# Kernel tuning notes

Measured on AMD Instinct MI355X. Metric: run time of the kernel, lower is better.

The kernel has to match this reference:

```python
import math
import jax, jax.numpy as jnp
import numpy as np

H = 64; W = 64; SX = 2; SY = 2; RATIO = 0.5; HEADS = 8


def _tome_indices(metric):
    # no_rand variant of bipartite_soft_matching_random2d: dst token is the
    # top-left element of every (SY, SX) block; indices computed under stop_gradient
    # (torch.no_grad in the original).
    m = jax.lax.stop_gradient(metric)
    B, N, _ = m.shape
    hsy, wsx = H // SY, W // SX
    num_dst = hsy * wsx
    dst_mask = ((jnp.arange(H)[:, None] % SY == 0) & (jnp.arange(W)[None, :] % SX == 0)).reshape(-1)
    order = jnp.argsort(jnp.where(dst_mask, -1, 0), stable=True)  # -1 entries (dst) first
    b_idx, a_idx = order[:num_dst], order[num_dst:]               # [num_dst], [N-num_dst]
    mn = m / jnp.linalg.norm(m, axis=-1, keepdims=True)
    a, b = mn[:, a_idx], mn[:, b_idx]
    scores = jnp.einsum('bsc,bdc->bsd', a, b)                      # [B, Ns, Nd] cosine sims
    r = min(a.shape[1], int(N * RATIO))
    node_max = scores.max(-1)
    node_idx = scores.argmax(-1)
    edge_idx = jnp.argsort(-node_max, axis=-1, stable=True)        # descending
    unm_idx, src_idx = edge_idx[:, r:], edge_idx[:, :r]
    dst_idx = jnp.take_along_axis(node_idx, src_idx, axis=1)
    return a_idx, b_idx, unm_idx, src_idx, dst_idx


def _merge(x, idxs):
    a_idx, b_idx, unm_idx, src_idx, dst_idx = idxs
    src, dst = x[:, a_idx], x[:, b_idx]
    unm = jnp.take_along_axis(src, unm_idx[..., None], axis=1)
    s = jnp.take_along_axis(src, src_idx[..., None], axis=1)
    bg = jnp.broadcast_to(jnp.arange(x.shape[0])[:, None], dst_idx.shape)
    sums = jnp.zeros_like(dst).at[bg, dst_idx].add(s)
    counts = jnp.zeros(dst.shape[:2], x.dtype).at[bg, dst_idx].add(1.0)
    dst = (dst + sums) / (1.0 + counts[..., None])  # scatter_reduce 'mean', include_self
    return jnp.concatenate([unm, dst], axis=1)


def _unmerge(x, idxs, N):
    a_idx, b_idx, unm_idx, src_idx, dst_idx = idxs
    unm_len = unm_idx.shape[1]
    unm, dst = x[:, :unm_len], x[:, unm_len:]
    s = jnp.take_along_axis(dst, dst_idx[..., None], axis=1)
    B, _, c = x.shape
    out = jnp.zeros((B, N, c), x.dtype)
    out = out.at[:, b_idx].set(dst)
    bgu = jnp.broadcast_to(jnp.arange(B)[:, None], unm_idx.shape)
    out = out.at[bgu, a_idx[unm_idx]].set(unm)
    bgs = jnp.broadcast_to(jnp.arange(B)[:, None], src_idx.shape)
    out = out.at[bgs, a_idx[src_idx]].set(s)
    return out


def _ln(x, g, b):
    mu = x.mean(-1, keepdims=True)
    var = ((x - mu) ** 2).mean(-1, keepdims=True)
    return (x - mu) / jnp.sqrt(var + 1e-5) * g + b


def _attn(x, ctx, wq, wk, wv, wo, bo):
    B, Nq, C = x.shape
    dh = C // HEADS
    q = (x @ wq).reshape(B, Nq, HEADS, dh)
    k = (ctx @ wk).reshape(B, -1, HEADS, dh)
    v = (ctx @ wv).reshape(B, -1, HEADS, dh)
    s = jnp.einsum('bqhd,bkhd->bhqk', q, k) * (1.0 / math.sqrt(dh))
    p = jax.nn.softmax(s, axis=-1)
    o = jnp.einsum('bhqk,bkhd->bqhd', p, v).reshape(B, Nq, C)
    return o @ wo + bo


def _forward(net, context, ln1_g, ln1_b, ln2_g, ln2_b, ln3_g, ln3_b,
             attn1_wq, attn1_wk, attn1_wv, attn1_wo, attn1_bo,
             attn2_wq, attn2_wk, attn2_wv, attn2_wo, attn2_bo,
             ff_w1, ff_b1, ff_w2, ff_b2):
    N = net.shape[1]
    idxs = _tome_indices(net)
    # self-attn with ToMe merge/unmerge (merge_attn=True)
    xm = _merge(_ln(net, ln1_g, ln1_b), idxs)
    net = _unmerge(_attn(xm, xm, attn1_wq, attn1_wk, attn1_wv, attn1_wo, attn1_bo), idxs, N) + net
    # cross-attn (merge_crossattn=False)
    net = _attn(_ln(net, ln2_g, ln2_b), context, attn2_wq, attn2_wk, attn2_wv, attn2_wo, attn2_bo) + net
    # GEGLU feed-forward (merge_mlp=False)
    h1 = _ln(net, ln3_g, ln3_b) @ ff_w1 + ff_b1
    xh, gh = jnp.split(h1, 2, axis=-1)
    net = (xh * jax.nn.gelu(gh, approximate=False)) @ ff_w2 + ff_b2 + net
    return net


def setup_inputs() -> dict:
    key = jax.random.key(0)
    ks = jax.random.split(key, 12)
    B, N, C, Lc, Dc = 2, 4096, 320, 77, 768
    dff = 4 * C
    w = lambda k, s: jax.random.normal(k, s, jnp.float32) * 0.02
    return {
        'net': jax.random.normal(ks[0], (B, N, C), jnp.float32),
        'context': jax.random.normal(ks[1], (B, Lc, Dc), jnp.float32),
        'ln1_g': jnp.ones((C,), jnp.float32), 'ln1_b': jnp.zeros((C,), jnp.float32),
        'ln2_g': jnp.ones((C,), jnp.float32), 'ln2_b': jnp.zeros((C,), jnp.float32),
        'ln3_g': jnp.ones((C,), jnp.float32), 'ln3_b': jnp.zeros((C,), jnp.float32),
        'attn1_wq': w(ks[2], (C, C)), 'attn1_wk': w(ks[3], (C, C)),
        'attn1_wv': w(ks[4], (C, C)), 'attn1_wo': w(ks[5], (C, C)),
        'attn1_bo': jnp.zeros((C,), jnp.float32),
        'attn2_wq': w(ks[6], (C, C)), 'attn2_wk': w(ks[7], (Dc, C)),
        'attn2_wv': w(ks[8], (Dc, C)), 'attn2_wo': w(ks[9], (C, C)),
        'attn2_bo': jnp.zeros((C,), jnp.float32),
        'ff_w1': w(ks[10], (C, 2 * dff)), 'ff_b1': jnp.zeros((2 * dff,), jnp.float32),
        'ff_w2': w(ks[11], (dff, C)), 'ff_b2': jnp.zeros((C,), jnp.float32),
    }


def reference(net, context, ln1_g, ln1_b, ln2_g, ln2_b, ln3_g, ln3_b,
              attn1_wq, attn1_wk, attn1_wv, attn1_wo, attn1_bo,
              attn2_wq, attn2_wk, attn2_wv, attn2_wo, attn2_bo,
              ff_w1, ff_b1, ff_w2, ff_b2):
    return _forward(net, context, ln1_g, ln1_b, ln2_g, ln2_b, ln3_g, ln3_b,
                    attn1_wq, attn1_wk, attn1_wv, attn1_wo, attn1_bo,
                    attn2_wq, attn2_wk, attn2_wv, attn2_wo, attn2_bo,
                    ff_w1, ff_b1, ff_w2, ff_b2)
```

## Files before the change

kernel.cpp:

```cpp
#include <hip/hip_runtime.h>

typedef __attribute__((ext_vector_type(8))) short bf16x8;
typedef __attribute__((ext_vector_type(4))) float f32x4;

constexpr int kB   = 2;
constexpr int kN   = 4096;
constexpr int kC   = 320;
constexpr int kNA  = 3072;
constexpr int kNB  = 1024;
constexpr int kNM  = 2048;
constexpr int kR   = 2048;
constexpr int kH   = 8;
constexpr int kDH  = 40;
constexpr int kLC  = 77;
constexpr int kDC  = 768;
constexpr int kDFF = 1280;

__device__ __forceinline__ unsigned short f2b(float f){
  unsigned u = __float_as_uint(f);
  u += 0x7FFF + ((u>>16)&1);
  return (unsigned short)(u>>16);
}
__device__ __forceinline__ float b2f(unsigned short h){ return __uint_as_float(((unsigned)h)<<16); }

__device__ __forceinline__ float wave_sum(float v){
  #pragma unroll
  for (int m=32;m>=1;m>>=1) v += __shfl_xor(v, m, 64);
  return v;
}
__device__ __forceinline__ int d_arank(int h, int w){
  int base = 32*((h+1)>>1) + 64*(h>>1);
  return base + ((h&1) ? w : (w>>1));
}

constexpr size_t rndB(size_t x){ return (x + 255) & ~(size_t)255; }
constexpr size_t B_mnA  = 0;
constexpr size_t B_mnB  = rndB(B_mnA + (size_t)kB*kNA*kC*4);
constexpr size_t B_y32  = rndB(B_mnB + (size_t)kB*kNB*kC*4);
constexpr size_t B_xm   = rndB(B_y32 + (size_t)kB*kN*kC*4);
constexpr size_t B_xo1  = rndB(B_xm  + (size_t)kB*kNM*kC*4);
constexpr size_t B_net1 = rndB(B_xo1 + (size_t)kB*kNM*kC*4);
constexpr size_t B_H    = 0;
constexpr size_t B_net2 = rndB(B_net1 + (size_t)kB*kN*kC*4);
constexpr size_t B_G    = rndB(B_net2 + (size_t)kB*kN*kC*4);
constexpr size_t B_QKb  = rndB(B_G    + (size_t)kB*kN*kDFF*2);
constexpr size_t B_Vtg  = rndB(B_QKb  + (size_t)kB*kNM*640*2);
constexpr size_t B_yb   = rndB(B_Vtg  + (size_t)320*kB*kNM*2);
constexpr size_t B_xmb  = rndB(B_yb   + (size_t)kB*kN*kC*2);
constexpr size_t B_Ao1b = rndB(B_xmb  + (size_t)kB*kNM*kC*2);
constexpr size_t B_Q2b  = rndB(B_Ao1b + (size_t)kB*kNM*kC*2);
constexpr size_t B_Ao2b = rndB(B_Q2b  + (size_t)kB*kN*kC*2);
constexpr size_t B_KV2b = rndB(B_Ao2b + (size_t)kB*kN*kC*2);
constexpr size_t B_Vt2g = rndB(B_KV2b + (size_t)kB*kLC*640*2);
constexpr size_t B_ctxb = rndB(B_Vt2g + (size_t)kB*320*80*2);
constexpr size_t B_Wqkv = rndB(B_ctxb + (size_t)kB*kLC*kDC*2);
constexpr size_t B_Wo1  = rndB(B_Wqkv + (size_t)960*320*2);
constexpr size_t B_Wq2  = rndB(B_Wo1  + (size_t)320*320*2);
constexpr size_t B_Wkv2 = rndB(B_Wq2  + (size_t)320*320*2);
constexpr size_t B_Wo2  = rndB(B_Wkv2 + (size_t)640*768*2);
constexpr size_t B_Wff1 = rndB(B_Wo2  + (size_t)320*320*2);
constexpr size_t B_Wff2 = rndB(B_Wff1 + (size_t)2560*320*2);
constexpr size_t B_cnt  = rndB(B_Wff2 + (size_t)320*1280*2);
constexpr size_t B_pack = rndB(B_cnt  + (size_t)kB*kNB*4);
constexpr size_t B_rank = rndB(B_pack + (size_t)kB*kNA*8);
constexpr size_t B_nidx = rndB(B_rank + (size_t)kB*kNA*4);
constexpr size_t B_mrg  = rndB(B_nidx + (size_t)kB*kNA*4);
constexpr size_t B_slot = rndB(B_mrg  + (size_t)kB*kNA*4);
constexpr size_t B_unml = rndB(B_slot + (size_t)kB*kNA*4);
constexpr size_t B_ucnt = rndB(B_unml + (size_t)kB*kNB*4);
constexpr size_t B_aidx = rndB(B_ucnt + 64);
constexpr size_t B_Op   = rndB(B_aidx + (size_t)kNA*4);
constexpr size_t B_lp   = rndB(B_Op   + (size_t)2*4096*320*4);

__global__ void k_gather(const float* __restrict__ net, float* __restrict__ mA, float* __restrict__ mB,
                         unsigned long long* __restrict__ pack, int* __restrict__ ucnt,
                         int* __restrict__ a_idx, int* __restrict__ rank){
  int blk = blockIdx.x; int b = blk >> 12; int t = blk & 4095;
  int lane = threadIdx.x;
  int gid = blk*64 + lane;
  if (gid < kB*kNA){ pack[gid] = 0ull; rank[gid] = 0; }
  if (gid < kB) ucnt[gid] = 0;
  if (gid < kN){
    int h = gid>>6, w = gid&63;
    if ((h|w)&1) a_idx[d_arank(h,w)] = gid;
  }
  const float* xp = net + ((size_t)b*kN + t)*kC;
  float v[5]; float s2 = 0.f;
  #pragma unroll
  for (int i=0;i<5;i++){ float f = xp[lane + i*64]; v[i]=f; s2 += f*f; }
  s2 = wave_sum(s2);
  float rn = 1.0f / sqrtf(s2);
  int h=t>>6, w=t&63;
  float* dp;
  if (!((h|w)&1)) dp = mB + ((size_t)b*kNB + ((h>>1)*32+(w>>1)))*kC;
  else            dp = mA + ((size_t)b*kNA + d_arank(h,w))*kC;
  #pragma unroll
  for (int i=0;i<5;i++) dp[lane + i*64] = v[i]*rn;
}

__global__ __launch_bounds__(256) void k_scores(const float* __restrict__ mA, const float* __restrict__ mB,
                                                unsigned long long* __restrict__ pack){
  __shared__ __align__(16) float As[16][136];
  __shared__ __align__(16) float Bs[16][68];
  const int b = blockIdx.z;
  const int m0 = blockIdx.x*128, n0 = blockIdx.y*64;
  const int tid = threadIdx.x;
  const int mr = tid>>4, nc = tid&15;
  const float* Ab = mA + (size_t)b*kNA*kC;
  const float* Bb = mB + (size_t)b*kNB*kC;
  float acc[8][4] = {};
  const int ar = tid>>1, ac8 = (tid&1)*8;
  const int br = tid>>2, bc4 = (tid&3)*4;
  for (int k0=0; k0<kC; k0+=16){
    __syncthreads();
    {
      float4 a0 = *reinterpret_cast<const float4*>(&Ab[(size_t)(m0+ar)*kC + k0 + ac8]);
      float4 a1 = *reinterpret_cast<const float4*>(&Ab[(size_t)(m0+ar)*kC + k0 + ac8 + 4]);
      As[ac8+0][ar]=a0.x; As[ac8+1][ar]=a0.y; As[ac8+2][ar]=a0.z; As[ac8+3][ar]=a0.w;
      As[ac8+4][ar]=a1.x; As[ac8+5][ar]=a1.y; As[ac8+6][ar]=a1.z; As[ac8+7][ar]=a1.w;
      float4 bv = *reinterpret_cast<const float4*>(&Bb[(size_t)(n0+br)*kC + k0 + bc4]);
      Bs[bc4+0][br]=bv.x; Bs[bc4+1][br]=bv.y; Bs[bc4+2][br]=bv.z; Bs[bc4+3][br]=bv.w;
    }
    __syncthreads();
    #pragma unroll
    for (int kk=0;kk<16;kk++){
      const float4 a4a = *reinterpret_cast<const float4*>(&As[kk][mr*8]);
      const float4 a4b = *reinterpret_cast<const float4*>(&As[kk][mr*8+4]);
      const float4 b4  = *reinterpret_cast<const float4*>(&Bs[kk][nc*4]);
      const float aa[8]={a4a.x,a4a.y,a4a.z,a4a.w,a4b.x,a4b.y,a4b.z,a4b.w};
      const float bb[4]={b4.x,b4.y,b4.z,b4.w};
      #pragma unroll
      for (int i=0;i<8;i++)
        #pragma unroll
        for (int j=0;j<4;j++)
          acc[i][j] = fmaf(aa[i], bb[j], acc[i][j]);
    }
  }
  #pragma unroll
  for (int i=0;i<8;i++){
    float bs = acc[i][0]; int bj = n0 + nc*4;
    #pragma unroll
    for (int j=1;j<4;j++){
      float v = acc[i][j];
      if (v > bs){ bs=v; bj=n0+nc*4+j; }
    }
    #pragma unroll
    for (int off=1; off<16; off<<=1){
      float os = __shfl_xor(bs, off, 16);
      int   oj = __shfl_xor(bj, off, 16);
      if (os > bs || (os == bs && oj < bj)){ bs=os; bj=oj; }
    }
    if (nc == 0){
      unsigned int u = __float_as_uint(bs);
      unsigned int key = (u & 0x80000000u) ? ~u : (u | 0x80000000u);
      unsigned long long pk = ((unsigned long long)key << 32) |
                              (unsigned long long)(0xFFFFFFFFu - (unsigned int)bj);
      atomicMax(&pack[(size_t)b*kNA + m0 + mr*8 + i], pk);
    }
  }
}
__global__ __launch_bounds__(256) void k_rank_part(const unsigned long long* __restrict__ pack,
                                                   int* __restrict__ rank){
  __shared__ unsigned int keys[256];
  const int b = blockIdx.z;
  const int i = blockIdx.x*256 + threadIdx.x;
  const int j0 = blockIdx.y*256;
  const unsigned long long* pb = pack + (size_t)b*kNA;
  keys[threadIdx.x] = (unsigned int)(pb[j0 + threadIdx.x]>>32);
  unsigned int ki = (unsigned int)(pb[i]>>32);
  __syncthreads();
  int cnt = 0;
  #pragma unroll 8
  for (int jj=0;jj<256;jj++){
    unsigned int kj = keys[jj];
    int j = j0 + jj;
    cnt += (kj > ki) || (kj == ki && j < i);
  }
  atomicAdd(&rank[(size_t)b*kNA + i], cnt);
}
__global__ void k_rank_assign(const unsigned long long* __restrict__ pack, const int* __restrict__ rank,
                              int* __restrict__ node_idx, int* __restrict__ merged,
                              int* __restrict__ slot_of, int* __restrict__ unm_list,
                              int* __restrict__ ucnt){
  int b = blockIdx.y;
  int i = blockIdx.x*256 + threadIdx.x;
  unsigned long long p = pack[(size_t)b*kNA + i];
  node_idx[(size_t)b*kNA + i] = (int)(0xFFFFFFFFu - (unsigned int)(p & 0xFFFFFFFFull));
  int mg = rank[(size_t)b*kNA + i] < kR;
  merged[(size_t)b*kNA + i] = mg;
  if (!mg){
    int s = atomicAdd(&ucnt[b], 1);
    unm_list[(size_t)b*kNB + s] = i;
    slot_of[(size_t)b*kNA + i] = s;
  }
}

template<bool OB>
__global__ void k_ln(const float* __restrict__ x, const float* __restrict__ g,
                     const float* __restrict__ be, void* __restrict__ yv){
  const int row = blockIdx.x;
  const int lane = threadIdx.x;
  const float* xp = x + (size_t)row*kC;
  float v[5]; float s=0.f, s2=0.f;
  #pragma unroll
  for (int i=0;i<5;i++){ float f = xp[lane + i*64]; v[i]=f; s+=f; s2+=f*f; }
  s = wave_sum(s); s2 = wave_sum(s2);
  float mu = s * (1.0f/kC);
  float var = s2 * (1.0f/kC) - mu*mu;
  float rstd = rsqrtf(var + 1e-5f);
  #pragma unroll
  for (int i=0;i<5;i++){
    int c = lane + i*64;
    float o = (v[i]-mu)*rstd*g[c] + be[c];
    if (OB) ((unsigned short*)yv)[(size_t)row*kC + c] = f2b(o);
    else    ((float*)yv)[(size_t)row*kC + c] = o;
  }
}

__global__ void k_merge_ud(const float* __restrict__ y, const int* __restrict__ a_idx,
                           const int* __restrict__ unm_list, unsigned short* __restrict__ xmb,
                           float* __restrict__ xm, float* __restrict__ cnt){
  int blk = blockIdx.x;
  int lane = threadIdx.x;
  if (blk < kB*kNB){
    int b = blk >> 10; int s = blk & 1023;
    int i = unm_list[(size_t)b*kNB + s];
    int t = a_idx[i];
    const float* sp = y + ((size_t)b*kN + t)*kC;
    unsigned short* dp = xmb + ((size_t)b*kNM + s)*kC;
    #pragma unroll
    for (int q=0;q<5;q++) dp[lane+q*64] = f2b(sp[lane+q*64]);
  } else {
    blk -= kB*kNB;
    int b = blk >> 10; int j = blk & 1023;
    int t = 128*(j>>5) + 2*(j&31);
    const float* sp = y + ((size_t)b*kN + t)*kC;
    float* dp = xm + ((size_t)b*kNM + kNB + j)*kC;
    #pragma unroll
    for (int q=0;q<5;q++) dp[lane+q*64] = sp[lane+q*64];
    if (lane==0) cnt[(size_t)b*kNB + j] = 1.0f;
  }
}
__global__ void k_merge_src(const float* __restrict__ y, const int* __restrict__ a_idx,
                            const int* __restrict__ merged, const int* __restrict__ node_idx,
                            float* __restrict__ xm, float* __restrict__ cnt){
  int blk = blockIdx.x; int b = blk / kNA; int i = blk % kNA;
  if (!merged[(size_t)b*kNA + i]) return;
  int t = a_idx[i]; int j = node_idx[(size_t)b*kNA + i];
  const float* sp = y + ((size_t)b*kN + t)*kC;
  float* dp = xm + ((size_t)b*kNM + kNB + j)*kC;
  int lane = threadIdx.x;
  #pragma unroll
  for (int q=0;q<5;q++) atomicAdd(&dp[lane+q*64], sp[lane+q*64]);
  if (lane==0) atomicAdd(&cnt[(size_t)b*kNB + j], 1.0f);
}
__global__ void k_merge_scale(const float* __restrict__ xm, const float* __restrict__ cnt,
                              unsigned short* __restrict__ xmb){
  int blk = blockIdx.x; int b = blk >> 10; int j = blk & 1023;
  float inv = 1.0f / cnt[(size_t)b*kNB + j];
  const float* sp = xm + ((size_t)b*kNM + kNB + j)*kC;
  unsigned short* dp = xmb + ((size_t)b*kNM + kNB + j)*kC;
  int lane = threadIdx.x;
  #pragma unroll
  for (int q=0;q<5;q++) dp[lane+q*64] = f2b(sp[lane+q*64]*inv);
}

__global__ __launch_bounds__(256) void k_wt_all(
    const float* __restrict__ w0, const float* __restrict__ w1, const float* __restrict__ w2,
    const float* __restrict__ w3, const float* __restrict__ w4, const float* __restrict__ w5,
    const float* __restrict__ w6, const float* __restrict__ w7, const float* __restrict__ w8,
    const float* __restrict__ w9,
    unsigned short* __restrict__ Wqkv, unsigned short* __restrict__ Wo1,
    unsigned short* __restrict__ Wq2,  unsigned short* __restrict__ Wkv2,
    unsigned short* __restrict__ Wo2,  unsigned short* __restrict__ Wff1,
    unsigned short* __restrict__ Wff2,
    const float* __restrict__ ctx, unsigned short* __restrict__ ctxb,
    unsigned short* __restrict__ Vt2){
  const int bid = blockIdx.x;
  const int tid = threadIdx.x;
  if (bid >= 570){
    int base = (bid-570)*2048 + tid*8;
    #pragma unroll
    for (int j=0;j<8;j++){
      int i = base + j;
      if (i < kB*kLC*kDC) ctxb[i] = f2b(ctx[i]);
    }
    if (bid == 570){
      for (int r=tid; r<kB*320; r+=256){
        Vt2[(size_t)r*80 + 77] = 0; Vt2[(size_t)r*80 + 78] = 0; Vt2[(size_t)r*80 + 79] = 0;
      }
    }
    return;
  }
  const int jb[11]   = {0,25,50,75,100,125,185,245,270,470,570};
  const float* srcs[10] = {w0,w1,w2,w3,w4,w5,w6,w7,w8,w9};
  unsigned short* dsts[10] = {Wqkv, Wqkv+320*320, Wqkv+640*320, Wo1, Wq2,
                              Wkv2, Wkv2+320*768, Wo2, Wff1, Wff2};
  const int Kd[10] = {320,320,320,320,320,768,768,320,320,1280};
  const int Nd[10] = {320,320,320,320,320,320,320,320,2560,320};
  int job = 0;
  while (bid >= jb[job+1]) job++;
  int local = bid - jb[job];
  const int Nt = (Nd[job]+63)>>6;
  int k0 = (local / Nt)*64, n0 = (local % Nt)*64;
  const float* W = srcs[job];
  unsigned short* Wt = dsts[job];
  const int K = Kd[job], N = Nd[job];
  __shared__ float tile[64][65];
  #pragma unroll
  for (int l=0;l<16;l++){
    int e = tid + l*256; int r = e>>6, c = e&63;
    int gk = k0+r, gn = n0+c;
    tile[r][c] = (gk<K && gn<N) ? W[(size_t)gk*N+gn] : 0.f;
  }
  __syncthreads();
  #pragma unroll
  for (int l=0;l<16;l++){
    int e = tid + l*256; int r = e>>6, c = e&63;
    int gn = n0+r, gk = k0+c;
    if (gn<N && gk<K) Wt[(size_t)gn*K+gk] = f2b(tile[c][r]);
  }
}

template<typename OT, bool BIAS, bool RES, int SVM>
__global__ __launch_bounds__(256) void k_bgemm(const unsigned short* __restrict__ A,
    const unsigned short* __restrict__ Bt, const float* __restrict__ bias,
    const float* __restrict__ resid, OT* __restrict__ out, unsigned short* __restrict__ vt,
    int M, int N, int K, int ldo){
  constexpr int LDK = 72;
  __shared__ unsigned short As[128*LDK];
  __shared__ unsigned short Bs[128*LDK];
  const int tid = threadIdx.x;
  const int m0 = blockIdx.x*128, n0 = blockIdx.y*128;
  const int wid = tid>>6, lane = tid&63;
  const int wm = (wid>>1)*64, wn = (wid&1)*64;
  const int lr = lane&15, quad = lane>>4;
  const f32x4 zero4 = {0.f,0.f,0.f,0.f};
  f32x4 acc[4][4];
  #pragma unroll
  for (int i=0;i<4;i++)
    #pragma unroll
    for (int j=0;j<4;j++) acc[i][j] = zero4;
  for (int k0=0; k0<K; k0+=64){
    __syncthreads();
    #pragma unroll
    for (int l=0;l<4;l++){
      int e = tid + l*256;
      int row = e>>3, seg = (e&7)*8;
      int gm = m0+row;
      uint4 va = (gm<M) ? *reinterpret_cast<const uint4*>(&A[(size_t)gm*K + k0 + seg])
                        : make_uint4(0u,0u,0u,0u);
      *reinterpret_cast<uint4*>(&As[row*LDK + seg]) = va;
      int gn = n0+row;
      uint4 vb = (gn<N) ? *reinterpret_cast<const uint4*>(&Bt[(size_t)gn*K + k0 + seg])
                        : make_uint4(0u,0u,0u,0u);
      *reinterpret_cast<uint4*>(&Bs[row*LDK + seg]) = vb;
    }
    __syncthreads();
    #pragma unroll
    for (int kk=0; kk<64; kk+=32){
      bf16x8 af[4], bfr[4];
      #pragma unroll
      for (int i=0;i<4;i++) af[i]  = *reinterpret_cast<const bf16x8*>(&As[(wm+i*16+lr)*LDK + kk + quad*8]);
      #pragma unroll
      for (int j=0;j<4;j++) bfr[j] = *reinterpret_cast<const bf16x8*>(&Bs[(wn+j*16+lr)*LDK + kk + quad*8]);
      #pragma unroll
      for (int i=0;i<4;i++)
        #pragma unroll
        for (int j=0;j<4;j++)
          acc[i][j] = __builtin_amdgcn_mfma_f32_16x16x32_bf16(af[i], bfr[j], acc[i][j], 0, 0, 0);
    }
  }
  #pragma unroll
  for (int i=0;i<4;i++){
    #pragma unroll
    for (int j=0;j<4;j++){
      int gn = n0 + wn + j*16 + lr;
      if (gn >= N) continue;
      float bv = BIAS ? bias[gn] : 0.f;
      #pragma unroll
      for (int r=0;r<4;r++){
        int gm = m0 + wm + i*16 + quad*4 + r;
        if (gm >= M) continue;
        float v = acc[i][j][r] + bv;
        if (RES) v += resid[(size_t)gm*ldo + gn];
        if (SVM == 1 && gn >= 640){
          vt[(size_t)(gn-640)*4096 + gm] = f2b(v);
        } else if (SVM == 2 && gn >= 320){
          int bb = gm / 77, tok = gm - bb*77;
          vt[((size_t)bb*320 + (gn-320))*80 + tok] = f2b(v);
        } else {
          if constexpr (sizeof(OT)==2) out[(size_t)gm*ldo + gn] = (OT)f2b(v);
          else                         out[(size_t)gm*ldo + gn] = (OT)v;
        }
      }
    }
  }
}

template<typename OT, bool BIAS, bool RES, int SVM>
__global__ __launch_bounds__(256) void k_bgemm64(const unsigned short* __restrict__ A,
    const unsigned short* __restrict__ Bt, const float* __restrict__ bias,
    const float* __restrict__ resid, OT* __restrict__ out, unsigned short* __restrict__ vt,
    int M, int N, int K, int ldo){
  constexpr int LDK = 72;
  __shared__ unsigned short As[64*LDK];
  __shared__ unsigned short Bs[64*LDK];
  const int tid = threadIdx.x;
  const int m0 = blockIdx.x*64, n0 = blockIdx.y*64;
  const int wid = tid>>6, lane = tid&63;
  const int wm = (wid>>1)*32, wn = (wid&1)*32;
  const int lr = lane&15, quad = lane>>4;
  const f32x4 zero4 = {0.f,0.f,0.f,0.f};
  f32x4 acc[2][2];
  #pragma unroll
  for (int i=0;i<2;i++)
    #pragma unroll
    for (int j=0;j<2;j++) acc[i][j] = zero4;
  for (int k0=0; k0<K; k0+=64){
    __syncthreads();
    #pragma unroll
    for (int l=0;l<2;l++){
      int e = tid + l*256;
      int row = e>>3, seg = (e&7)*8;
      int gm = m0+row;
      uint4 va = (gm<M) ? *reinterpret_cast<const uint4*>(&A[(size_t)gm*K + k0 + seg])
                        : make_uint4(0u,0u,0u,0u);
      *reinterpret_cast<uint4*>(&As[row*LDK + seg]) = va;
      int gn = n0+row;
      uint4 vb = (gn<N) ? *reinterpret_cast<const uint4*>(&Bt[(size_t)gn*K + k0 + seg])
                        : make_uint4(0u,0u,0u,0u);
      *reinterpret_cast<uint4*>(&Bs[row*LDK + seg]) = vb;
    }
    __syncthreads();
    #pragma unroll
    for (int kk=0; kk<64; kk+=32){
      bf16x8 af[2], bfr[2];
      #pragma unroll
      for (int i=0;i<2;i++) af[i]  = *reinterpret_cast<const bf16x8*>(&As[(wm+i*16+lr)*LDK + kk + quad*8]);
      #pragma unroll
      for (int j=0;j<2;j++) bfr[j] = *reinterpret_cast<const bf16x8*>(&Bs[(wn+j*16+lr)*LDK + kk + quad*8]);
      #pragma unroll
      for (int i=0;i<2;i++)
        #pragma unroll
        for (int j=0;j<2;j++)
          acc[i][j] = __builtin_amdgcn_mfma_f32_16x16x32_bf16(af[i], bfr[j], acc[i][j], 0, 0, 0);
    }
  }
  #pragma unroll
  for (int i=0;i<2;i++){
    #pragma unroll
    for (int j=0;j<2;j++){
      int gn = n0 + wn + j*16 + lr;
      if (gn >= N) continue;
      float bv = BIAS ? bias[gn] : 0.f;
      #pragma unroll
      for (int r=0;r<4;r++){
        int gm = m0 + wm + i*16 + quad*4 + r;
        if (gm >= M) continue;
        float v = acc[i][j][r] + bv;
        if (RES) v += resid[(size_t)gm*ldo + gn];
        if (SVM == 1 && gn >= 640){
          vt[(size_t)(gn-640)*4096 + gm] = f2b(v);
        } else if (SVM == 2 && gn >= 320){
          int bb = gm / 77, tok = gm - bb*77;
          vt[((size_t)bb*320 + (gn-320))*80 + tok] = f2b(v);
        } else {
          if constexpr (sizeof(OT)==2) out[(size_t)gm*ldo + gn] = (OT)f2b(v);
          else                         out[(size_t)gm*ldo + gn] = (OT)v;
        }
      }
    }
  }
}

__global__ void k_geglu(const unsigned short* __restrict__ H, unsigned short* __restrict__ G){
  int e = blockIdx.x*256 + threadIdx.x;
  int m = e/160, t = e - m*160;
  const unsigned short* hp = H + (size_t)m*2560 + t*8;
  uint4 xv = *reinterpret_cast<const uint4*>(hp);
  uint4 gv = *reinterpret_cast<const uint4*>(hp + 1280);
  const unsigned short* xu = reinterpret_cast<const unsigned short*>(&xv);
  const unsigned short* gu = reinterpret_cast<const unsigned short*>(&gv);
  unsigned short ov[8];
  #pragma unroll
  for (int d=0; d<8; d++){
    float x = b2f(xu[d]);
    float g = b2f(gu[d]);
    float ge = 0.5f*g*(1.0f + erff(g*0.70710678118654752f));
    ov[d] = f2b(x*ge);
  }
  *reinterpret_cast<uint4*>(G + (size_t)m*1280 + t*8) = *reinterpret_cast<const uint4*>(ov);
}

__global__ __launch_bounds__(256) void k_attn1(const unsigned short* __restrict__ QK,
                                               const unsigned short* __restrict__ Vtg,
                                               float* __restrict__ Opart,
                                               float* __restrict__ lpart){
  constexpr int LP = 72, LV = 136;
  __shared__ unsigned short Ks[128*LP];
  __shared__ unsigned short Vt[48*LV];
  __shared__ unsigned short Ps[64*LV];
  const int b = blockIdx.z, hh = blockIdx.y;
  const int bx = blockIdx.x;
  const int q0 = (bx>>1)*64, kz = bx&1;
  const int tid = threadIdx.x;
  const int wid = tid>>6, lane = tid&63;
  const int lr = lane&15, quad = lane>>4;
  const int wm = wid*16;
  const float scale = 0.15811388300841898f;
  const unsigned short* Kb = QK + ((size_t)b*kNM)*640 + 320 + hh*kDH;
  const unsigned short* Vb = Vtg + (size_t)hh*kDH*4096 + (size_t)b*kNM;
  const uint4 z4 = make_uint4(0u,0u,0u,0u);
  const unsigned short* Qrow = QK + ((size_t)b*kNM + q0 + wm + lr)*640 + hh*kDH;
  bf16x8 aq0 = *reinterpret_cast<const bf16x8*>(Qrow + quad*8);
  bf16x8 aq1 = {0,0,0,0,0,0,0,0};
  if (quad == 0) aq1 = *reinterpret_cast<const bf16x8*>(Qrow + 32);
  for (int e=tid; e<384; e+=256){
    int row=e/3, seg=40+(e%3)*8;
    *reinterpret_cast<uint4*>(&Ks[row*LP+seg]) = z4;
  }
  for (int e=tid; e<136; e+=256){
    int row=40+e/17, seg=(e%17)*8;
    *reinterpret_cast<uint4*>(&Vt[row*LV+seg]) = z4;
  }
  const f32x4 zf = {0.f,0.f,0.f,0.f};
  f32x4 oacc[3] = {zf, zf, zf};
  float l_i[4] = {0.f, 0.f, 0.f, 0.f};
  const int kbeg = kz*1024, kend = kbeg + 1024;
  for (int kt=kbeg; kt<kend; kt+=128){
    __syncthreads();
    for (int e=tid; e<640; e+=256){
      int row=e/5, seg=(e%5)*8;
      *reinterpret_cast<uint4*>(&Ks[row*LP+seg]) =
        *reinterpret_cast<const uint4*>(Kb + (size_t)(kt+row)*640 + seg);
    }
    for (int e=tid; e<640; e+=256){
      int d=e>>4, seg=(e&15)*8;
      *reinterpret_cast<uint4*>(&Vt[d*LV+seg]) =
        *reinterpret_cast<const uint4*>(Vb + (size_t)d*4096 + kt + seg);
    }
    __syncthreads();
    f32x4 sacc[8];
    #pragma unroll
    for (int j=0;j<8;j++){
      bf16x8 bk0 = *reinterpret_cast<const bf16x8*>(&Ks[(j*16+lr)*LP + quad*8]);
      sacc[j] = __builtin_amdgcn_mfma_f32_16x16x32_bf16(aq0, bk0, zf, 0,0,0);
      bf16x8 bk1 = *reinterpret_cast<const bf16x8*>(&Ks[(j*16+lr)*LP + 32 + quad*8]);
      sacc[j] = __builtin_amdgcn_mfma_f32_16x16x32_bf16(aq1, bk1, sacc[j], 0,0,0);
    }
    #pragma unroll
    for (int r=0;r<4;r++){
      int row = wm + quad*4 + r;
      float psum = 0.f;
      #pragma unroll
      for (int j=0;j<8;j++){
        float p = __expf(sacc[j][r]*scale);
        psum += p;
        Ps[row*LV + j*16 + lr] = f2b(p);
      }
      #pragma unroll
      for (int off=1; off<16; off<<=1) psum += __shfl_xor(psum, off, 64);
      l_i[r] += psum;
    }
    #pragma unroll
    for (int s=0;s<4;s++){
      bf16x8 ap = *reinterpret_cast<const bf16x8*>(&Ps[(wm+lr)*LV + s*32 + quad*8]);
      #pragma unroll
      for (int nt=0;nt<3;nt++){
        bf16x8 bv = *reinterpret_cast<const bf16x8*>(&Vt[(nt*16+lr)*LV + s*32 + quad*8]);
        oacc[nt] = __builtin_amdgcn_mfma_f32_16x16x32_bf16(ap, bv, oacc[nt], 0,0,0);
      }
    }
  }
  float* Op = Opart + (size_t)kz*4096*320;
  float* lp = lpart + (size_t)kz*4096*8;
  #pragma unroll
  for (int r=0;r<4;r++){
    int grow = b*kNM + q0 + wm + quad*4 + r;
    #pragma unroll
    for (int nt=0;nt<3;nt++){
      int d = nt*16 + lr;
      if (d < kDH) Op[(size_t)grow*320 + hh*kDH + d] = oacc[nt][r];
    }
    if (lr == 0) lp[(size_t)grow*8 + hh] = l_i[r];
  }
}

__global__ void k_acomb(const float* __restrict__ Opart, const float* __restrict__ lpart,
                        unsigned short* __restrict__ Ao1b){
  int row = blockIdx.x;
  int lane = threadIdx.x;
  const float* o0 = Opart + (size_t)row*320;
  const float* o1 = Opart + (size_t)2*4096*320/2 + (size_t)row*320;
  const float* l0 = lpart + (size_t)row*8;
  const float* l1 = lpart + (size_t)4096*8 + (size_t)row*8;
  #pragma unroll
  for (int i=0;i<5;i++){
    int c = lane + i*64;
    int h = c/kDH;
    float v = (o0[c] + o1[c]) / (l0[h] + l1[h]);
    Ao1b[(size_t)row*320 + c] = f2b(v);
  }
}

__global__ __launch_bounds__(256) void k_attn2m(const unsigned short* __restrict__ Q,
                                                const unsigned short* __restrict__ KV,
                                                const unsigned short* __restrict__ Vt2,
                                                unsigned short* __restrict__ Oa){
  constexpr int LP = 72, LP2 = 104;
  __shared__ unsigned short Qs[64*LP];
  __shared__ unsigned short Ks[80*LP];
  __shared__ unsigned short Vts[48*LP2];
  __shared__ unsigned short Ps[64*LP2];
  const int b = blockIdx.z, hh = blockIdx.y;
  const int q0 = blockIdx.x*64;
  const int tid = threadIdx.x;
  const int wid = tid>>6, lane = tid&63;
  const int lr = lane&15, quad = lane>>4;
  const int wm = wid*16;
  const float scale = 0.15811388300841898f;
  const uint4 z4 = make_uint4(0u,0u,0u,0u);
  for (int e=tid; e<576; e+=256) *reinterpret_cast<uint4*>(&Qs[e*8]) = z4;
  for (int e=tid; e<720; e+=256) *reinterpret_cast<uint4*>(&Ks[e*8]) = z4;
  for (int e=tid; e<624; e+=256) *reinterpret_cast<uint4*>(&Vts[e*8]) = z4;
  for (int e=tid; e<832; e+=256) *reinterpret_cast<uint4*>(&Ps[e*8]) = z4;
  __syncthreads();
  for (int e=tid; e<320; e+=256){
    int row=e/5, seg=(e%5)*8;
    *reinterpret_cast<uint4*>(&Qs[row*LP+seg]) =
      *reinterpret_cast<const uint4*>(Q + ((size_t)b*kN + q0 + row)*kC + hh*kDH + seg);
  }
  for (int e=tid; e<385; e+=256){
    int row=e/5, seg=(e%5)*8;
    *reinterpret_cast<uint4*>(&Ks[row*LP+seg]) =
      *reinterpret_cast<const uint4*>(KV + ((size_t)b*kLC + row)*640 + hh*kDH + seg);
  }
  for (int e=tid; e<400; e+=256){
    int d=e/10, seg=(e%10)*8;
    *reinterpret_cast<uint4*>(&Vts[d*LP2+seg]) =
      *reinterpret_cast<const uint4*>(Vt2 + ((size_t)b*320 + hh*kDH + d)*80 + seg);
  }
  __syncthreads();
  const f32x4 zf = {0.f,0.f,0.f,0.f};
  f32x4 sacc[5] = {zf, zf, zf, zf, zf};
  bf16x8 aq0 = *reinterpret_cast<const bf16x8*>(&Qs[(wm+lr)*LP + quad*8]);
  bf16x8 aq1 = *reinterpret_cast<const bf16x8*>(&Qs[(wm+lr)*LP + 32 + quad*8]);
  #pragma unroll
  for (int j=0;j<5;j++){
    bf16x8 bk0 = *reinterpret_cast<const bf16x8*>(&Ks[(j*16+lr)*LP + quad*8]);
    sacc[j] = __builtin_amdgcn_mfma_f32_16x16x32_bf16(aq0, bk0, sacc[j], 0,0,0);
    bf16x8 bk1 = *reinterpret_cast<const bf16x8*>(&Ks[(j*16+lr)*LP + 32 + quad*8]);
    sacc[j] = __builtin_amdgcn_mfma_f32_16x16x32_bf16(aq1, bk1, sacc[j], 0,0,0);
  }
  float l_i[4];
  #pragma unroll
  for (int r=0;r<4;r++){
    float vv[5];
    float rm = -1e30f;
    #pragma unroll
    for (int j=0;j<5;j++){
      int c = j*16 + lr;
      vv[j] = sacc[j][r]*scale;
      if (c < kLC) rm = fmaxf(rm, vv[j]);
    }
    #pragma unroll
    for (int off=1; off<16; off<<=1) rm = fmaxf(rm, __shfl_xor(rm, off, 64));
    float psum = 0.f;
    int row = wm + quad*4 + r;
    #pragma unroll
    for (int j=0;j<5;j++){
      int c = j*16 + lr;
      float p = (c < kLC) ? __expf(vv[j]-rm) : 0.f;
      psum += p;
      Ps[row*LP2 + c] = f2b(p);
    }
    #pragma unroll
    for (int off=1; off<16; off<<=1) psum += __shfl_xor(psum, off, 64);
    l_i[r] = psum;
  }
  f32x4 oacc[3] = {zf, zf, zf};
  #pragma unroll
  for (int s=0;s<3;s++){
    bf16x8 ap = *reinterpret_cast<const bf16x8*>(&Ps[(wm+lr)*LP2 + s*32 + quad*8]);
    #pragma unroll
    for (int nt=0;nt<3;nt++){
      bf16x8 bv = *reinterpret_cast<const bf16x8*>(&Vts[(nt*16+lr)*LP2 + s*32 + quad*8]);
      oacc[nt] = __builtin_amdgcn_mfma_f32_16x16x32_bf16(ap, bv, oacc[nt], 0,0,0);
    }
  }
  #pragma unroll
  for (int r=0;r<4;r++){
    float inv = 1.0f / l_i[r];
    unsigned short* Ob = Oa + ((size_t)b*kN + q0 + wm + quad*4 + r)*kC + hh*kDH;
    #pragma unroll
    for (int nt=0;nt<3;nt++){
      int d = nt*16 + lr;
      if (d < kDH) Ob[d] = f2b(oacc[nt][r]*inv);
    }
  }
}

__global__ void k_unmerge(const float* __restrict__ net, const float* __restrict__ Xo,
                          const int* __restrict__ merged, const int* __restrict__ node_idx,
                          const int* __restrict__ slot_of, float* __restrict__ net1){
  int blk = blockIdx.x; int b = blk >> 12; int t = blk & 4095;
  int h = t>>6, w = t&63;
  int row;
  if (!((h|w)&1)) row = kNB + ((h>>1)*32 + (w>>1));
  else {
    int i = d_arank(h,w);
    row = merged[(size_t)b*kNA+i] ? (kNB + node_idx[(size_t)b*kNA+i]) : slot_of[(size_t)b*kNA+i];
  }
  const float* np_ = net + ((size_t)b*kN + t)*kC;
  const float* xp = Xo + ((size_t)b*kNM + row)*kC;
  float* op = net1 + ((size_t)b*kN + t)*kC;
  int lane = threadIdx.x;
  #pragma unroll
  for (int q=0;q<5;q++){ int c = lane+q*64; op[c] = np_[c] + xp[c]; }
}

extern "C" void kernel_launch(void* const* d_in, const int* in_sizes, int n_in,
                              void* d_out, int out_size, void* d_ws, size_t ws_size,
                              hipStream_t stream){
  const float* net = (const float*)d_in[0];
  const float* ctx = (const float*)d_in[1];
  const float* ln1g=(const float*)d_in[2], *ln1b=(const float*)d_in[3];
  const float* ln2g=(const float*)d_in[4], *ln2b=(const float*)d_in[5];
  const float* ln3g=(const float*)d_in[6], *ln3b=(const float*)d_in[7];
  const float* w1q=(const float*)d_in[8],  *w1k=(const float*)d_in[9];
  const float* w1v=(const float*)d_in[10], *w1o=(const float*)d_in[11];
  const float* b1o=(const float*)d_in[12];
  const float* w2q=(const float*)d_in[13], *w2k=(const float*)d_in[14];
  const float* w2v=(const float*)d_in[15], *w2o=(const float*)d_in[16];
  const float* b2o=(const float*)d_in[17];
  const float* fw1=(const float*)d_in[18], *fb1=(const float*)d_in[19];
  const float* fw2=(const float*)d_in[20], *fb2=(const float*)d_in[21];

  char* ws = (char*)d_ws;
  float* mnA  = (float*)(ws + B_mnA);
  float* mnB  = (float*)(ws + B_mnB);
  float* y32  = (float*)(ws + B_y32);
  float* xm32 = (float*)(ws + B_xm);
  float* Xo1  = (float*)(ws + B_xo1);
  float* net1 = (float*)(ws + B_net1);
  float* net2 = (float*)(ws + B_net2);
  float* cnt  = (float*)(ws + B_cnt);
  unsigned short* Hb   = (unsigned short*)(ws + B_H);
  unsigned short* Gb   = (unsigned short*)(ws + B_G);
  unsigned short* QKb  = (unsigned short*)(ws + B_QKb);
  unsigned short* Vtg  = (unsigned short*)(ws + B_Vtg);
  unsigned short* yb   = (unsigned short*)(ws + B_yb);
  unsigned short* xmb  = (unsigned short*)(ws + B_xmb);
  unsigned short* Ao1b = (unsigned short*)(ws + B_Ao1b);
  unsigned short* Q2b  = (unsigned short*)(ws + B_Q2b);
  unsigned short* Ao2b = (unsigned short*)(ws + B_Ao2b);
  unsigned short* KV2b = (unsigned short*)(ws + B_KV2b);
  unsigned short* Vt2g = (unsigned short*)(ws + B_Vt2g);
  unsigned short* ctxb = (unsigned short*)(ws + B_ctxb);
  unsigned short* Wqkv = (unsigned short*)(ws + B_Wqkv);
  unsigned short* Wo1  = (unsigned short*)(ws + B_Wo1);
  unsigned short* Wq2  = (unsigned short*)(ws + B_Wq2);
  unsigned short* Wkv2 = (unsigned short*)(ws + B_Wkv2);
  unsigned short* Wo2  = (unsigned short*)(ws + B_Wo2);
  unsigned short* Wff1 = (unsigned short*)(ws + B_Wff1);
  unsigned short* Wff2 = (unsigned short*)(ws + B_Wff2);
  unsigned long long* pack = (unsigned long long*)(ws + B_pack);
  int* rnk  = (int*)(ws + B_rank);
  int* nidx = (int*)(ws + B_nidx); int* mrg = (int*)(ws + B_mrg); int* slot = (int*)(ws + B_slot);
  int* unml = (int*)(ws + B_unml); int* ucnt = (int*)(ws + B_ucnt); int* aidx = (int*)(ws + B_aidx);
  float* Opart = (float*)(ws + B_Op);
  float* lpart = (float*)(ws + B_lp);

  k_wt_all<<<628, 256, 0, stream>>>(w1q, w1k, w1v, w1o, w2q, w2k, w2v, w2o, fw1, fw2,
                                    Wqkv, Wo1, Wq2, Wkv2, Wo2, Wff1, Wff2, ctx, ctxb, Vt2g);

  k_gather<<<kB*kN, 64, 0, stream>>>(net, mnA, mnB, pack, ucnt, aidx, rnk);
  k_scores<<<dim3(kNA/128, kNB/64, kB), 256, 0, stream>>>(mnA, mnB, pack);
  k_rank_part  <<<dim3(kNA/256, kNA/256, kB), 256, 0, stream>>>(pack, rnk);
  k_rank_assign<<<dim3(kNA/256, kB), 256, 0, stream>>>(pack, rnk, nidx, mrg, slot, unml, ucnt);
  k_ln<false><<<kB*kN, 64, 0, stream>>>(net, ln1g, ln1b, y32);
  k_merge_ud   <<<kB*kNB*2, 64, 0, stream>>>(y32, aidx, unml, xmb, xm32, cnt);
  k_merge_src  <<<kB*kNA, 64, 0, stream>>>(y32, aidx, mrg, nidx, xm32, cnt);
  k_merge_scale<<<kB*kNB, 64, 0, stream>>>(xm32, cnt, xmb);
  k_bgemm64<unsigned short,false,false,1><<<dim3(64,15), 256, 0, stream>>>(
      xmb, Wqkv, nullptr, nullptr, QKb, Vtg, 4096, 960, 320, 640);
  k_attn1<<<dim3((kNM/64)*2, kH, kB), 256, 0, stream>>>(QKb, Vtg, Opart, lpart);
  k_acomb<<<kB*kNM, 64, 0, stream>>>(Opart, lpart, Ao1b);
  k_bgemm64<float,true,false,0><<<dim3(64,5), 256, 0, stream>>>(
      Ao1b, Wo1, b1o, nullptr, Xo1, nullptr, 4096, 320, 320, 320);
  k_unmerge<<<kB*kN, 64, 0, stream>>>(net, Xo1, mrg, nidx, slot, net1);
  k_ln<true><<<kB*kN, 64, 0, stream>>>(net1, ln2g, ln2b, yb);
  k_bgemm64<unsigned short,false,false,0><<<dim3(128,5), 256, 0, stream>>>(
      yb, Wq2, nullptr, nullptr, Q2b, nullptr, 8192, 320, 320, 320);
  k_bgemm<unsigned short,false,false,2><<<dim3(2,5), 256, 0, stream>>>(
      ctxb, Wkv2, nullptr, nullptr, KV2b, Vt2g, 154, 640, 768, 640);
  k_attn2m<<<dim3(kN/64, kH, kB), 256, 0, stream>>>(Q2b, KV2b, Vt2g, Ao2b);
  k_bgemm64<float,true,true,0><<<dim3(128,5), 256, 0, stream>>>(
      Ao2b, Wo2, b2o, net1, net2, nullptr, 8192, 320, 320, 320);
  k_ln<true><<<kB*kN, 64, 0, stream>>>(net2, ln3g, ln3b, yb);
  k_bgemm<unsigned short,true,false,0><<<dim3(64,20), 256, 0, stream>>>(
      yb, Wff1, fb1, nullptr, Hb, nullptr, 8192, 2560, 320, 2560);
  k_geglu<<<(kB*kN*160+255)/256, 256, 0, stream>>>(Hb, Gb);
  k_bgemm64<float,true,true,0><<<dim3(128,5), 256, 0, stream>>>(
      Gb, Wff2, fb2, net2, (float*)d_out, nullptr, 8192, 320, 1280, 320);
}
```

Measured before the change: 490.9 us.

## Remove split-K in self-attention and normalize output in-kernel

```diff
diff --git a/kernel.cpp b/kernel.cpp
--- a/kernel.cpp
+++ b/kernel.cpp
@@ -69,8 +69,6 @@
 constexpr size_t B_unml = rndB(B_slot + (size_t)kB*kNA*4);
 constexpr size_t B_ucnt = rndB(B_unml + (size_t)kB*kNB*4);
 constexpr size_t B_aidx = rndB(B_ucnt + 64);
-constexpr size_t B_Op   = rndB(B_aidx + (size_t)kNA*4);
-constexpr size_t B_lp   = rndB(B_Op   + (size_t)2*4096*320*4);
 
 __global__ void k_gather(const float* __restrict__ net, float* __restrict__ mA, float* __restrict__ mB,
                          unsigned long long* __restrict__ pack, int* __restrict__ ucnt,
@@ -495,15 +493,13 @@
 
 __global__ __launch_bounds__(256) void k_attn1(const unsigned short* __restrict__ QK,
                                                const unsigned short* __restrict__ Vtg,
-                                               float* __restrict__ Opart,
-                                               float* __restrict__ lpart){
+                                               unsigned short* __restrict__ Oa){
   constexpr int LP = 72, LV = 136;
   __shared__ unsigned short Ks[128*LP];
   __shared__ unsigned short Vt[48*LV];
   __shared__ unsigned short Ps[64*LV];
   const int b = blockIdx.z, hh = blockIdx.y;
-  const int bx = blockIdx.x;
-  const int q0 = (bx>>1)*64, kz = bx&1;
+  const int q0 = blockIdx.x*64;
   const int tid = threadIdx.x;
   const int wid = tid>>6, lane = tid&63;
   const int lr = lane&15, quad = lane>>4;
@@ -527,8 +523,7 @@
   const f32x4 zf = {0.f,0.f,0.f,0.f};
   f32x4 oacc[3] = {zf, zf, zf};
   float l_i[4] = {0.f, 0.f, 0.f, 0.f};
-  const int kbeg = kz*1024, kend = kbeg + 1024;
-  for (int kt=kbeg; kt<kend; kt+=128){
+  for (int kt=0; kt<kNM; kt+=128){
     __syncthreads();
     for (int e=tid; e<640; e+=256){
       int row=e/5, seg=(e%5)*8;
@@ -573,34 +568,15 @@
       }
     }
   }
-  float* Op = Opart + (size_t)kz*4096*320;
-  float* lp = lpart + (size_t)kz*4096*8;
   #pragma unroll
   for (int r=0;r<4;r++){
-    int grow = b*kNM + q0 + wm + quad*4 + r;
+    float inv = 1.0f / l_i[r];
+    unsigned short* Ob = Oa + ((size_t)b*kNM + q0 + wm + quad*4 + r)*kC + hh*kDH;
     #pragma unroll
     for (int nt=0;nt<3;nt++){
       int d = nt*16 + lr;
-      if (d < kDH) Op[(size_t)grow*320 + hh*kDH + d] = oacc[nt][r];
-    }
-    if (lr == 0) lp[(size_t)grow*8 + hh] = l_i[r];
-  }
-}
-
-__global__ void k_acomb(const float* __restrict__ Opart, const float* __restrict__ lpart,
-                        unsigned short* __restrict__ Ao1b){
-  int row = blockIdx.x;
-  int lane = threadIdx.x;
-  const float* o0 = Opart + (size_t)row*320;
-  const float* o1 = Opart + (size_t)2*4096*320/2 + (size_t)row*320;
-  const float* l0 = lpart + (size_t)row*8;
-  const float* l1 = lpart + (size_t)4096*8 + (size_t)row*8;
-  #pragma unroll
-  for (int i=0;i<5;i++){
-    int c = lane + i*64;
-    int h = c/kDH;
-    float v = (o0[c] + o1[c]) / (l0[h] + l1[h]);
-    Ao1b[(size_t)row*320 + c] = f2b(v);
+      if (d < kDH) Ob[d] = f2b(oacc[nt][r]*inv);
+    }
   }
 }
 
@@ -769,8 +745,6 @@
   int* rnk  = (int*)(ws + B_rank);
   int* nidx = (int*)(ws + B_nidx); int* mrg = (int*)(ws + B_mrg); int* slot = (int*)(ws + B_slot);
   int* unml = (int*)(ws + B_unml); int* ucnt = (int*)(ws + B_ucnt); int* aidx = (int*)(ws + B_aidx);
-  float* Opart = (float*)(ws + B_Op);
-  float* lpart = (float*)(ws + B_lp);
 
   k_wt_all<<<628, 256, 0, stream>>>(w1q, w1k, w1v, w1o, w2q, w2k, w2v, w2o, fw1, fw2,
                                     Wqkv, Wo1, Wq2, Wkv2, Wo2, Wff1, Wff2, ctx, ctxb, Vt2g);
@@ -785,8 +759,7 @@
   k_merge_scale<<<kB*kNB, 64, 0, stream>>>(xm32, cnt, xmb);
   k_bgemm64<unsigned short,false,false,1><<<dim3(64,15), 256, 0, stream>>>(
       xmb, Wqkv, nullptr, nullptr, QKb, Vtg, 4096, 960, 320, 640);
-  k_attn1<<<dim3((kNM/64)*2, kH, kB), 256, 0, stream>>>(QKb, Vtg, Opart, lpart);
-  k_acomb<<<kB*kNM, 64, 0, stream>>>(Opart, lpart, Ao1b);
+  k_attn1<<<dim3(kNM/64, kH, kB), 256, 0, stream>>>(QKb, Vtg, Ao1b);
   k_bgemm64<float,true,false,0><<<dim3(64,5), 256, 0, stream>>>(
       Ao1b, Wo1, b1o, nullptr, Xo1, nullptr, 4096, 320, 320, 320);
   k_unmerge<<<kB*kN, 64, 0, stream>>>(net, Xo1, mrg, nidx, slot, net1);
```

Measured after the change: 470.6 us. -4.1%, faster.
